# Performance work log

Measured on AMD Instinct MI355X. Metric: run time of the kernel, lower is better.

Reference implementation:

```python
import jax, jax.numpy as jnp
import numpy as np

B = 100000      # query points
L = 8           # num levels
N_RBF = 256     # RBF centers per level
F = 16          # features per level
OUT = 3         # output dim


def setup_inputs() -> dict:
    key = jax.random.key(0)
    k = jax.random.split(key, 6)
    x = jax.random.normal(k[0], (B, 3), dtype=jnp.float32)
    # small-magnitude features so gaussian RBF responses are non-degenerate
    feats = 0.1 * jax.random.normal(k[1], (B, L * F), dtype=jnp.float32)
    # centers initialized uniform(-1e-4, 1e-4) as in the torch module
    centers = jax.random.uniform(k[2], (L, N_RBF, F), dtype=jnp.float32,
                                 minval=-1e-4, maxval=1e-4)
    # log-width parameters (exp'd in forward); small perturbation around 0
    betas = 0.01 * jax.random.normal(k[3], (L, N_RBF, F), dtype=jnp.float32)
    W = jax.random.normal(k[4], (OUT, N_RBF * L), dtype=jnp.float32) / np.sqrt(N_RBF * L)
    b = jax.random.normal(k[5], (OUT,), dtype=jnp.float32) * 0.01
    return {"x": x, "feats": feats, "centers": centers, "betas": betas, "W": W, "b": b}


def reference(x, feats, centers, betas, W, b):
    # centers, betas: [L, N, F]. x is unused by the original forward (faithful).
    Lnum, N, f = centers.shape
    rbfs = []
    for i in range(Lnum):
        # concat of first i+1 per-level tables along feature axis -> [N, (i+1)*f]
        C = centers[: i + 1].transpose(1, 0, 2).reshape(N, (i + 1) * f)
        Bw = jnp.exp(betas[: i + 1].transpose(1, 0, 2).reshape(N, (i + 1) * f))
        x_in = feats[:, : (i + 1) * f]                      # [B, (i+1)*f]
        term1 = (x_in * x_in) @ Bw.T                        # [B, N]
        term2 = x_in @ (Bw * C).T                           # [B, N]
        term3 = jnp.sum(Bw * C * C, axis=1)                 # [N]
        dist_sq = term1 - 2.0 * term2 + term3[None, :]
        rbfs.append(jnp.exp(-0.5 * dist_sq))                # gaussian basis
    outs = jnp.concatenate(rbfs, axis=-1)                   # [B, L*N]
    return outs @ W.T + b
```

## Files before the change

kernel.cpp:

```cpp
#include <hip/hip_runtime.h>
#include <math.h>

#define LN 8
#define NRBF 256
#define FD 16
#define OUTD 3
#define KC (-0.72134752044f)

typedef __attribute__((ext_vector_type(8))) short short8;
typedef __attribute__((ext_vector_type(4))) float floatx4;
typedef __attribute__((ext_vector_type(2))) float floatx2;

__device__ __forceinline__ short f2bf(float f) {
    unsigned u = __builtin_bit_cast(unsigned, f);
    u += 0x7fffu + ((u >> 16) & 1u);
    return (short)(u >> 16);
}


__global__ __launch_bounds__(256) void prep(
    const float* __restrict__ centers, const float* __restrict__ betas,
    const float* __restrict__ W, short* __restrict__ PKB, float* __restrict__ EPI)
{
    __shared__ float ls[LN * 32];
    int blk = blockIdx.x;
    int tid = threadIdx.x;
    if (blk < 32) {
        int t = blk * 256 + tid;
        int lane = t & 63;
        int nt   = (t >> 6) & 15;
        int j    = t >> 10;
        int n    = nt * 16 + (lane & 15);
        int kq   = lane >> 4;
        size_t base = ((size_t)(j * NRBF + n)) * FD + kq * 4;
        float4 bq = *(const float4*)(betas + base);
        float4 cq = *(const float4*)(centers + base);
        float a0 = __expf(bq.x), a1 = __expf(bq.y), a2 = __expf(bq.z), a3 = __expf(bq.w);
        short8 v;
        v[0] = f2bf(a0); v[1] = f2bf(-2.0f * a0 * cq.x);
        v[2] = f2bf(a1); v[3] = f2bf(-2.0f * a1 * cq.y);
        v[4] = f2bf(a2); v[5] = f2bf(-2.0f * a2 * cq.z);
        v[6] = f2bf(a3); v[7] = f2bf(-2.0f * a3 * cq.w);
        *((short8*)(PKB + (size_t)t * 8)) = v;
    } else {
        int jj = tid >> 5;
        int nl = tid & 31;
        int n  = (blk - 32) * 32 + nl;
        const float* bp = betas   + ((size_t)(jj * NRBF + n)) * FD;
        const float* cp = centers + ((size_t)(jj * NRBF + n)) * FD;
        float s = 0.f;
#pragma unroll
        for (int q = 0; q < 4; ++q) {
            float4 bq = *(const float4*)(bp + q * 4);
            float4 cq = *(const float4*)(cp + q * 4);
            s = fmaf(__expf(bq.x) * cq.x, cq.x, s);
            s = fmaf(__expf(bq.y) * cq.y, cq.y, s);
            s = fmaf(__expf(bq.z) * cq.z, cq.z, s);
            s = fmaf(__expf(bq.w) * cq.w, cq.w, s);
        }
        ls[jj * 32 + nl] = s;
        __syncthreads();
        float t3 = 0.f;
        for (int j2 = 0; j2 <= jj; ++j2) t3 += ls[j2 * 32 + nl];
        float4 e;
        e.x = KC * t3;
        e.y = W[0 * (LN * NRBF) + jj * NRBF + n];
        e.z = W[1 * (LN * NRBF) + jj * NRBF + n];
        e.w = W[2 * (LN * NRBF) + jj * NRBF + n];
        int nt = n >> 4, l = n & 15;
        ((float4*)EPI)[(jj * 16 + nt) * 16 + l] = e;
    }
}

__global__ __launch_bounds__(256, 3) void rbf_mfma(
    const float* __restrict__ feats, const short* __restrict__ PKB,
    const float* __restrict__ EPI, const float* __restrict__ bias,
    float* __restrict__ out, int B)
{
    __shared__ short8 pk_s[2][16 * 64];
    __shared__ float4 ep_s[2][16 * 16];

    int tid  = threadIdx.x;
    int lane = tid & 63;
    int w    = tid >> 6;
    int ntile_total = (B + 15) >> 4;
    int tile = blockIdx.x * 4 + w;
    bool tvalid = (tile < ntile_total);
    if (!tvalid) tile = ntile_total - 1;
    int b0 = tile * 16;
    int m  = lane & 15;
    int kq = lane >> 4;

    int brow = b0 + m; if (brow >= B) brow = B - 1;
    const float* xrow = feats + (size_t)brow * (LN * FD) + kq * 4;
    short8 afrag[LN];
#pragma unroll
    for (int j = 0; j < LN; ++j) {
        float4 x = *((const float4*)(xrow + j * FD));
        short8 f;
        f[0] = f2bf(x.x * x.x); f[1] = f2bf(x.x);
        f[2] = f2bf(x.y * x.y); f[3] = f2bf(x.y);
        f[4] = f2bf(x.z * x.z); f[5] = f2bf(x.z);
        f[6] = f2bf(x.w * x.w); f[7] = f2bf(x.w);
        afrag[j] = f;
    }

#define STAGE(buf, jv)                                                          \
    do {                                                                        \
        _Pragma("unroll")                                                       \
        for (int i = 0; i < 4; ++i) {                                           \
            const short* gp = PKB + ((size_t)(jv) * 1024 + (w * 4 + i) * 64 + lane) * 8; \
            __builtin_amdgcn_global_load_lds(                                   \
                (const __attribute__((address_space(1))) void*)gp,              \
                (__attribute__((address_space(3))) void*)&pk_s[buf][(w * 4 + i) * 64], \
                16, 0, 0);                                                      \
        }                                                                       \
        const float* ge = EPI + ((size_t)(jv) * 256 + w * 64 + lane) * 4;       \
        __builtin_amdgcn_global_load_lds(                                       \
            (const __attribute__((address_space(1))) void*)ge,                  \
            (__attribute__((address_space(3))) void*)&ep_s[buf][w * 64],        \
            16, 0, 0);                                                          \
    } while (0)

    floatx4 acc[16];
#pragma unroll
    for (int nt = 0; nt < 16; ++nt) acc[nt] = (floatx4){0.f, 0.f, 0.f, 0.f};

    floatx2 o01[4];
    float   o2[4];
#pragma unroll
    for (int r = 0; r < 4; ++r) { o01[r] = (floatx2){0.f, 0.f}; o2[r] = 0.f; }

    STAGE(0, 0);
    __syncthreads();

#pragma unroll
    for (int j = 0; j < LN; ++j) {
        int cur = j & 1;
        if (j < LN - 1) STAGE(cur ^ 1, j + 1);

#pragma unroll
        for (int nt = 0; nt < 16; ++nt) {
            short8 bf = pk_s[cur][nt * 64 + lane];
            acc[nt] = __builtin_amdgcn_mfma_f32_16x16x32_bf16(afrag[j], bf, acc[nt], 0, 0, 0);
        }

#pragma unroll
        for (int nt = 0; nt < 16; ++nt) {
            float4 e = ep_s[cur][nt * 16 + m];
            floatx2 eyz = {e.y, e.z};
#pragma unroll
            for (int r = 0; r < 4; ++r) {
                float rv = __builtin_amdgcn_exp2f(fmaf(acc[nt][r], KC, e.x));
                o01[r] += (floatx2){rv, rv} * eyz;
                o2[r]   = fmaf(rv, e.w, o2[r]);
            }
        }
        __syncthreads();
    }
#undef STAGE

    float oacc[12];
#pragma unroll
    for (int r = 0; r < 4; ++r) {
        oacc[r * 3 + 0] = o01[r].x;
        oacc[r * 3 + 1] = o01[r].y;
        oacc[r * 3 + 2] = o2[r];
    }
#pragma unroll
    for (int i = 0; i < 12; ++i) {
        oacc[i] += __shfl_xor(oacc[i], 1);
        oacc[i] += __shfl_xor(oacc[i], 2);
        oacc[i] += __shfl_xor(oacc[i], 4);
        oacc[i] += __shfl_xor(oacc[i], 8);
    }

    if (tvalid && m < OUTD) {
        float bv = bias[m];
#pragma unroll
        for (int r = 0; r < 4; ++r) {
            int row = b0 + kq * 4 + r;
            if (row < B) out[(size_t)row * OUTD + m] = oacc[r * 3 + m] + bv;
        }
    }
}

extern "C" void kernel_launch(void* const* d_in, const int* in_sizes, int n_in,
                              void* d_out, int out_size, void* d_ws, size_t ws_size,
                              hipStream_t stream) {
    const float* feats   = (const float*)d_in[1];
    const float* centers = (const float*)d_in[2];
    const float* betas   = (const float*)d_in[3];
    const float* W       = (const float*)d_in[4];
    const float* bias    = (const float*)d_in[5];
    float* out = (float*)d_out;
    int B = in_sizes[1] / (LN * FD);

    short* PKB = (short*)d_ws;
    float* EPI = (float*)((char*)d_ws + 65536 * 2);

    prep<<<40, 256, 0, stream>>>(centers, betas, W, PKB, EPI);

    int tiles  = (B + 15) / 16;
    int blocks = (tiles + 3) / 4;
    rbf_mfma<<<blocks, 256, 0, stream>>>(feats, PKB, EPI, bias, out, B);
}
```

Before: 143.3 us.

## Swap loop order to RBF-tile outer, fold exp constants into prep tables

The main loop now iterates over RBF-center tiles on the outside and levels on the inside, so a single running MFMA accumulator replaces sixteen. Each level's partial sum is exponentiated and projected as soon as it is ready, overlapping with the next MFMA. The -0.5/ln2 scale is folded into the packed B operand and exp(-term3) into the projection weights, which removes an FMA per element and packs the third output into paired float2 ops. The risk is that exp2 of the bf16-scaled product loses precision and the staging now needs sixteen syncs instead of eight.

```diff
diff --git a/kernel.cpp b/kernel.cpp
--- a/kernel.cpp
+++ b/kernel.cpp
@@ -26,22 +26,23 @@
     int blk = blockIdx.x;
     int tid = threadIdx.x;
     if (blk < 32) {
-        int t = blk * 256 + tid;
-        int lane = t & 63;
-        int nt   = (t >> 6) & 15;
-        int j    = t >> 10;
+        int g    = blk * 256 + tid;
+        int lane = g & 63;
+        int j    = (g >> 6) & 7;
+        int nt   = g >> 9;
         int n    = nt * 16 + (lane & 15);
         int kq   = lane >> 4;
         size_t base = ((size_t)(j * NRBF + n)) * FD + kq * 4;
         float4 bq = *(const float4*)(betas + base);
         float4 cq = *(const float4*)(centers + base);
-        float a0 = __expf(bq.x), a1 = __expf(bq.y), a2 = __expf(bq.z), a3 = __expf(bq.w);
+        float a0 = KC * __expf(bq.x), a1 = KC * __expf(bq.y);
+        float a2 = KC * __expf(bq.z), a3 = KC * __expf(bq.w);
         short8 v;
         v[0] = f2bf(a0); v[1] = f2bf(-2.0f * a0 * cq.x);
         v[2] = f2bf(a1); v[3] = f2bf(-2.0f * a1 * cq.y);
         v[4] = f2bf(a2); v[5] = f2bf(-2.0f * a2 * cq.z);
         v[6] = f2bf(a3); v[7] = f2bf(-2.0f * a3 * cq.w);
-        *((short8*)(PKB + (size_t)t * 8)) = v;
+        *((short8*)(PKB + (size_t)g * 8)) = v;
     } else {
         int jj = tid >> 5;
         int nl = tid & 31;
@@ -62,110 +63,130 @@
         __syncthreads();
         float t3 = 0.f;
         for (int j2 = 0; j2 <= jj; ++j2) t3 += ls[j2 * 32 + nl];
+        float E = __builtin_amdgcn_exp2f(KC * t3);
         float4 e;
-        e.x = KC * t3;
-        e.y = W[0 * (LN * NRBF) + jj * NRBF + n];
-        e.z = W[1 * (LN * NRBF) + jj * NRBF + n];
-        e.w = W[2 * (LN * NRBF) + jj * NRBF + n];
-        int nt = n >> 4, l = n & 15;
-        ((float4*)EPI)[(jj * 16 + nt) * 16 + l] = e;
-    }
-}
-
-__global__ __launch_bounds__(256, 3) void rbf_mfma(
+        e.x = W[0 * (LN * NRBF) + jj * NRBF + n] * E;
+        e.y = W[1 * (LN * NRBF) + jj * NRBF + n] * E;
+        e.z = W[2 * (LN * NRBF) + jj * NRBF + n] * E;
+        e.w = 0.f;
+        ((float4*)EPI)[((size_t)(n >> 4) * 128) + jj * 16 + (n & 15)] = e;
+    }
+}
+
+#define CVT(dst, vv)  do {                                         \
+        short8 f_;                                                 \
+        f_[0] = f2bf((vv).x * (vv).x); f_[1] = f2bf((vv).x);       \
+        f_[2] = f2bf((vv).y * (vv).y); f_[3] = f2bf((vv).y);       \
+        f_[4] = f2bf((vv).z * (vv).z); f_[5] = f2bf((vv).z);       \
+        f_[6] = f2bf((vv).w * (vv).w); f_[7] = f2bf((vv).w);       \
+        (dst) = f_; } while (0)
+
+__global__ __launch_bounds__(256) void rbf_mfma(
     const float* __restrict__ feats, const short* __restrict__ PKB,
     const float* __restrict__ EPI, const float* __restrict__ bias,
     float* __restrict__ out, int B)
 {
-    __shared__ short8 pk_s[2][16 * 64];
-    __shared__ float4 ep_s[2][16 * 16];
+    __shared__ short8 pk_s[2][8 * 64];
+    __shared__ float4 ep_s[2][8 * 16];
 
     int tid  = threadIdx.x;
     int lane = tid & 63;
     int w    = tid >> 6;
-    int ntile_total = (B + 15) >> 4;
+    int ntile = (B + 15) >> 4;
     int tile = blockIdx.x * 4 + w;
-    bool tvalid = (tile < ntile_total);
-    if (!tvalid) tile = ntile_total - 1;
+    bool tvalid = (tile < ntile);
+    if (!tvalid) tile = ntile - 1;
     int b0 = tile * 16;
     int m  = lane & 15;
     int kq = lane >> 4;
-
     int brow = b0 + m; if (brow >= B) brow = B - 1;
     const float* xrow = feats + (size_t)brow * (LN * FD) + kq * 4;
-    short8 afrag[LN];
-#pragma unroll
-    for (int j = 0; j < LN; ++j) {
-        float4 x = *((const float4*)(xrow + j * FD));
-        short8 f;
-        f[0] = f2bf(x.x * x.x); f[1] = f2bf(x.x);
-        f[2] = f2bf(x.y * x.y); f[3] = f2bf(x.y);
-        f[4] = f2bf(x.z * x.z); f[5] = f2bf(x.z);
-        f[6] = f2bf(x.w * x.w); f[7] = f2bf(x.w);
-        afrag[j] = f;
-    }
-
-#define STAGE(buf, jv)                                                          \
+
+#define STAGE(buf, ntv)                                                         \
     do {                                                                        \
         _Pragma("unroll")                                                       \
-        for (int i = 0; i < 4; ++i) {                                           \
-            const short* gp = PKB + ((size_t)(jv) * 1024 + (w * 4 + i) * 64 + lane) * 8; \
+        for (int q = 0; q < 2; ++q) {                                           \
+            const short* gp = PKB + ((size_t)(ntv) * 512 + w * 128 + q * 64 + lane) * 8; \
             __builtin_amdgcn_global_load_lds(                                   \
                 (const __attribute__((address_space(1))) void*)gp,              \
-                (__attribute__((address_space(3))) void*)&pk_s[buf][(w * 4 + i) * 64], \
+                (__attribute__((address_space(3))) void*)&pk_s[buf][w * 128 + q * 64], \
                 16, 0, 0);                                                      \
         }                                                                       \
-        const float* ge = EPI + ((size_t)(jv) * 256 + w * 64 + lane) * 4;       \
-        __builtin_amdgcn_global_load_lds(                                       \
-            (const __attribute__((address_space(1))) void*)ge,                  \
-            (__attribute__((address_space(3))) void*)&ep_s[buf][w * 64],        \
-            16, 0, 0);                                                          \
+        if (lane < 32) {                                                        \
+            const float* ge = EPI + ((size_t)(ntv) * 128 + w * 32 + lane) * 4;  \
+            __builtin_amdgcn_global_load_lds(                                   \
+                (const __attribute__((address_space(1))) void*)ge,              \
+                (__attribute__((address_space(3))) void*)&ep_s[buf][w * 32],    \
+                16, 0, 0);                                                      \
+        }                                                                       \
     } while (0)
 
-    floatx4 acc[16];
-#pragma unroll
-    for (int nt = 0; nt < 16; ++nt) acc[nt] = (floatx4){0.f, 0.f, 0.f, 0.f};
+#define EXPPROJ(accv, ev)                                          \
+    do {                                                           \
+        floatx2 exy_ = { (ev).x, (ev).y };                         \
+        floatx2 ezz_ = { (ev).z, (ev).z };                         \
+        float rv0_ = __builtin_amdgcn_exp2f((accv)[0]);            \
+        float rv1_ = __builtin_amdgcn_exp2f((accv)[1]);            \
+        float rv2_ = __builtin_amdgcn_exp2f((accv)[2]);            \
+        float rv3_ = __builtin_amdgcn_exp2f((accv)[3]);            \
+        o01[0] += (floatx2){rv0_, rv0_} * exy_;                    \
+        o01[1] += (floatx2){rv1_, rv1_} * exy_;                    \
+        o01[2] += (floatx2){rv2_, rv2_} * exy_;                    \
+        o01[3] += (floatx2){rv3_, rv3_} * exy_;                    \
+        oz[0]  += (floatx2){rv0_, rv1_} * ezz_;                    \
+        oz[1]  += (floatx2){rv2_, rv3_} * ezz_;                    \
+    } while (0)
+
+    STAGE(0, 0);
+
+    short8 af[LN];
+#pragma unroll
+    for (int j = 0; j < LN; ++j) {
+        float4 xa = *(const float4*)(xrow + j * FD);
+        CVT(af[j], xa);
+    }
 
     floatx2 o01[4];
-    float   o2[4];
-#pragma unroll
-    for (int r = 0; r < 4; ++r) { o01[r] = (floatx2){0.f, 0.f}; o2[r] = 0.f; }
-
-    STAGE(0, 0);
+    floatx2 oz[2];
+#pragma unroll
+    for (int r = 0; r < 4; ++r) o01[r] = (floatx2){0.f, 0.f};
+    oz[0] = (floatx2){0.f, 0.f}; oz[1] = (floatx2){0.f, 0.f};
+
     __syncthreads();
 
-#pragma unroll
-    for (int j = 0; j < LN; ++j) {
-        int cur = j & 1;
-        if (j < LN - 1) STAGE(cur ^ 1, j + 1);
-
-#pragma unroll
-        for (int nt = 0; nt < 16; ++nt) {
-            short8 bf = pk_s[cur][nt * 64 + lane];
-            acc[nt] = __builtin_amdgcn_mfma_f32_16x16x32_bf16(afrag[j], bf, acc[nt], 0, 0, 0);
-        }
-
-#pragma unroll
-        for (int nt = 0; nt < 16; ++nt) {
-            float4 e = ep_s[cur][nt * 16 + m];
-            floatx2 eyz = {e.y, e.z};
-#pragma unroll
-            for (int r = 0; r < 4; ++r) {
-                float rv = __builtin_amdgcn_exp2f(fmaf(acc[nt][r], KC, e.x));
-                o01[r] += (floatx2){rv, rv} * eyz;
-                o2[r]   = fmaf(rv, e.w, o2[r]);
+#pragma unroll 1
+    for (int nt = 0; nt < 16; ++nt) {
+        int cur = nt & 1;
+        if (nt < 15) STAGE(cur ^ 1, nt + 1);
+
+        floatx4 acc = (floatx4){0.f, 0.f, 0.f, 0.f};
+        floatx4 accp;
+
+#pragma unroll
+        for (int j = 0; j < LN; ++j) {
+            short8 bf = pk_s[cur][j * 64 + lane];
+            acc = __builtin_amdgcn_mfma_f32_16x16x32_bf16(af[j], bf, acc, 0, 0, 0);
+            if (j > 0) {
+                float4 e = ep_s[cur][(j - 1) * 16 + m];
+                EXPPROJ(accp, e);
             }
+            accp = acc;
+        }
+        {
+            float4 e = ep_s[cur][7 * 16 + m];
+            EXPPROJ(accp, e);
         }
         __syncthreads();
     }
 #undef STAGE
+#undef EXPPROJ
 
     float oacc[12];
 #pragma unroll
     for (int r = 0; r < 4; ++r) {
         oacc[r * 3 + 0] = o01[r].x;
         oacc[r * 3 + 1] = o01[r].y;
-        oacc[r * 3 + 2] = o2[r];
+        oacc[r * 3 + 2] = (r & 1) ? oz[r >> 1].y : oz[r >> 1].x;
     }
 #pragma unroll
     for (int i = 0; i < 12; ++i) {
```

Result: faster. 140.0 us, median of 2 (-2.3%).
